# Kernel tuning notes

Hardware: AMD Instinct MI355X
Metric: run time of the kernel (lower is better)

Reference implementation:

```python
import jax, jax.numpy as jnp
import numpy as np

B, S, D, H = 2, 2048, 2048, 16
DH = D // H
FF = 4 * D
EPS = 1e-5


def setup_inputs() -> dict:
    key = jax.random.key(0)
    ks = jax.random.split(key, 8)
    sd = 0.02
    return {
        "hidden_states": jax.random.normal(ks[0], (B, S, D), jnp.float32),
        "ln1_w": jnp.ones((D,), jnp.float32),
        "ln1_b": jnp.zeros((D,), jnp.float32),
        "qkv_w": jax.random.normal(ks[1], (3 * D, D), jnp.float32) * sd,
        "qkv_b": jnp.zeros((3 * D,), jnp.float32),
        "dense_w": jax.random.normal(ks[2], (D, D), jnp.float32) * sd,
        "dense_b": jnp.zeros((D,), jnp.float32),
        "ln2_w": jnp.ones((D,), jnp.float32),
        "ln2_b": jnp.zeros((D,), jnp.float32),
        "fc1_w": jax.random.normal(ks[3], (FF, D), jnp.float32) * sd,
        "fc1_b": jnp.zeros((FF,), jnp.float32),
        "fc2_w": jax.random.normal(ks[4], (D, FF), jnp.float32) * sd,
        "fc2_b": jnp.zeros((D,), jnp.float32),
    }


def _layer_norm(x, w, b):
    mu = jnp.mean(x, axis=-1, keepdims=True)
    var = jnp.mean(jnp.square(x - mu), axis=-1, keepdims=True)
    return (x - mu) * jax.lax.rsqrt(var + EPS) * w + b


def _attention(x, qkv_w, qkv_b, dense_w, dense_b):
    qkv = x @ qkv_w.T + qkv_b  # [B,S,3D]
    q, k, v = jnp.split(qkv, 3, axis=-1)
    q = q.reshape(B, S, H, DH)
    k = k.reshape(B, S, H, DH)
    v = v.reshape(B, S, H, DH)
    scale = DH ** -0.5
    scores = jnp.einsum("bqhd,bkhd->bhqk", q, k) * scale
    causal = jnp.tril(jnp.ones((S, S), bool))
    scores = jnp.where(causal, scores, jnp.finfo(scores.dtype).min)
    probs = jax.nn.softmax(scores, axis=-1)
    out = jnp.einsum("bhqk,bkhd->bqhd", probs, v).reshape(B, S, D)
    return out @ dense_w.T + dense_b


def reference(hidden_states, ln1_w, ln1_b, qkv_w, qkv_b, dense_w, dense_b,
              ln2_w, ln2_b, fc1_w, fc1_b, fc2_w, fc2_b):
    residual = hidden_states
    x = _layer_norm(hidden_states, ln1_w, ln1_b)
    x = _attention(x, qkv_w, qkv_b, dense_w, dense_b) + residual
    residual = x
    h = _layer_norm(x, ln2_w, ln2_b)
    h = jax.nn.gelu(h @ fc1_w.T + fc1_b, approximate=False)
    h = h @ fc2_w.T + fc2_b
    return residual + h
```

## Files before the change

### kernel.cpp

```cpp
#include <hip/hip_runtime.h>
#include <hip/hip_bf16.h>

#define SEQ    2048
#define DMODEL 2048
#define NHEAD  16
#define DHEAD  128
#define TOK    4096
#define TD     6144
#define FFDIM  8192

typedef __attribute__((ext_vector_type(4)))  float f32x4;
typedef __attribute__((ext_vector_type(16))) float f32x16;
typedef __attribute__((ext_vector_type(8)))  short short8v;

__device__ __forceinline__ void async_ld16(const void* src, void* lds) {
  __builtin_amdgcn_global_load_lds((const __attribute__((address_space(1))) void*)src,
                                   (__attribute__((address_space(3))) void*)lds, 16, 0, 0);
}

__device__ __forceinline__ unsigned pk2(float a, float b) {
  union { __hip_bfloat16 h[2]; unsigned u; } p;
  p.h[0] = __float2bfloat16(a);
  p.h[1] = __float2bfloat16(b);
  return p.u;
}

__global__ __launch_bounds__(256) void f2bf_kernel(const float* __restrict__ in,
                                                   __hip_bfloat16* __restrict__ out, long n) {
  long i0 = ((long)blockIdx.x * 256 + threadIdx.x) * 8;
  long stride = (long)gridDim.x * 256 * 8;
  for (long i = i0; i < n; i += stride) {
    float4 a = *(const float4*)(in + i);
    float4 b = *(const float4*)(in + i + 4);
    union { __hip_bfloat16 h[8]; int4 v; } p;
    p.h[0] = __float2bfloat16(a.x); p.h[1] = __float2bfloat16(a.y);
    p.h[2] = __float2bfloat16(a.z); p.h[3] = __float2bfloat16(a.w);
    p.h[4] = __float2bfloat16(b.x); p.h[5] = __float2bfloat16(b.y);
    p.h[6] = __float2bfloat16(b.z); p.h[7] = __float2bfloat16(b.w);
    *(int4*)(out + i) = p.v;
  }
}

__global__ __launch_bounds__(256) void ln_kernel(const float* __restrict__ x,
                                                 const float* __restrict__ w,
                                                 const float* __restrict__ b,
                                                 __hip_bfloat16* __restrict__ out) {
  __shared__ float red[8];
  const int row = blockIdx.x;
  const int tid = threadIdx.x;
  const float* xr = x + (long)row * DMODEL;
  float4 v0 = ((const float4*)xr)[tid * 2];
  float4 v1 = ((const float4*)xr)[tid * 2 + 1];
  float s  = v0.x + v0.y + v0.z + v0.w + v1.x + v1.y + v1.z + v1.w;
  float ss = v0.x*v0.x + v0.y*v0.y + v0.z*v0.z + v0.w*v0.w
           + v1.x*v1.x + v1.y*v1.y + v1.z*v1.z + v1.w*v1.w;
  #pragma unroll
  for (int m = 1; m < 64; m <<= 1) { s += __shfl_xor(s, m, 64); ss += __shfl_xor(ss, m, 64); }
  if ((tid & 63) == 0) { red[tid >> 6] = s; red[4 + (tid >> 6)] = ss; }
  __syncthreads();
  s  = red[0] + red[1] + red[2] + red[3];
  ss = red[4] + red[5] + red[6] + red[7];
  const float mu = s * (1.0f / DMODEL);
  const float rs = rsqrtf(ss * (1.0f / DMODEL) - mu * mu + 1e-5f);
  float4 w0 = ((const float4*)w)[tid * 2], w1 = ((const float4*)w)[tid * 2 + 1];
  float4 b0 = ((const float4*)b)[tid * 2], b1 = ((const float4*)b)[tid * 2 + 1];
  union { __hip_bfloat16 h[8]; int4 v; } p;
  p.h[0] = __float2bfloat16((v0.x - mu) * rs * w0.x + b0.x);
  p.h[1] = __float2bfloat16((v0.y - mu) * rs * w0.y + b0.y);
  p.h[2] = __float2bfloat16((v0.z - mu) * rs * w0.z + b0.z);
  p.h[3] = __float2bfloat16((v0.w - mu) * rs * w0.w + b0.w);
  p.h[4] = __float2bfloat16((v1.x - mu) * rs * w1.x + b1.x);
  p.h[5] = __float2bfloat16((v1.y - mu) * rs * w1.y + b1.y);
  p.h[6] = __float2bfloat16((v1.z - mu) * rs * w1.z + b1.z);
  p.h[7] = __float2bfloat16((v1.w - mu) * rs * w1.w + b1.w);
  ((int4*)(out + (long)row * DMODEL))[tid] = p.v;
}

#define G2_BAR()    asm volatile("s_barrier" ::: "memory")
#define G2_BARLG()  asm volatile("s_barrier\ns_waitcnt lgkmcnt(0)" ::: "memory")
#define G2_VM4()    asm volatile("s_waitcnt vmcnt(4)\ns_barrier" ::: "memory")
#define G2_VM0()    asm volatile("s_waitcnt vmcnt(0)\ns_barrier" ::: "memory")

#define READ_A(BB, MH) \
  _Pragma("unroll") \
  for (int m = 0; m < 4; ++m) { \
    int row = wr * 128 + (MH) * 64 + m * 16 + l15; \
    _Pragma("unroll") \
    for (int kk = 0; kk < 2; ++kk) \
      af[m][kk] = *(const short8v*)((BB) + row * 128 + ((((kk << 2) | c16) ^ (row & 7)) << 4)); \
  }
#define MFMA_BLK(MH, NB) \
  __builtin_amdgcn_s_setprio(1); \
  _Pragma("unroll") \
  for (int m = 0; m < 4; ++m) \
    _Pragma("unroll") \
    for (int n = 0; n < 2; ++n) \
      _Pragma("unroll") \
      for (int kk = 0; kk < 2; ++kk) \
        acc[(MH) * 4 + m][(NB) + n] = __builtin_amdgcn_mfma_f32_16x16x32_bf16( \
            af[m][kk], bf[(NB) + n][kk], acc[(MH) * 4 + m][(NB) + n], 0, 0, 0); \
  __builtin_amdgcn_s_setprio(0);

#define READ_B128(BB) \
  _Pragma("unroll") \
  for (int n = 0; n < 2; ++n) { \
    int row = wc * 32 + n * 16 + l15; \
    _Pragma("unroll") \
    for (int kk = 0; kk < 2; ++kk) \
      bf[n][kk] = *(const short8v*)((BB) + 32768 + row * 128 + ((((kk << 2) | c16) ^ (row & 7)) << 4)); \
  }

template <int MODE>
__global__ __launch_bounds__(512, 2) void gemm128n(const __hip_bfloat16* __restrict__ A,
                                                   const __hip_bfloat16* __restrict__ B,
                                                   const float* __restrict__ bias,
                                                   const float* __restrict__ resid,
                                                   void* __restrict__ outp,
                                                   int N, long K) {
  __shared__ __align__(16) char lds[98304];
  const int tid = threadIdx.x;
  const int lane = tid & 63, w = tid >> 6;
  const int wr = w >> 2, wc = w & 3;
  const int l15 = lane & 15, c16 = lane >> 4;
  const int gx = gridDim.x;
  const int nwg = gx * (int)gridDim.y;
  const int lin = (int)blockIdx.y * gx + (int)blockIdx.x;
  const int cpx = nwg >> 3;
  const int swz = (lin & 7) * cpx + (lin >> 3);
  const long m0 = (long)(swz / gx) * 256;
  const long n0 = (long)(swz % gx) * 128;
  const int NT = (int)(K >> 6);
  const int NI = NT >> 1;

  auto stA2 = [&](int t, int par) {
    char* base = lds + (t & 1) * 49152;
    #pragma unroll
    for (int j = 0; j < 2; ++j) {
      int q = 2 * j + par;
      int row = q * 64 + (tid >> 3);
      long col = (long)t * 64 + (((tid & 7) ^ (row & 7)) << 3);
      async_ld16(A + (m0 + row) * K + col, base + q * 8192 + w * 1024);
    }
  };
  auto stB1 = [&](int t) {
    char* base = lds + (t & 1) * 49152 + 32768;
    #pragma unroll
    for (int j = 0; j < 2; ++j) {
      int row = j * 64 + (tid >> 3);
      long col = (long)t * 64 + (((tid & 7) ^ (row & 7)) << 3);
      async_ld16(B + (n0 + row) * K + col, base + j * 8192 + w * 1024);
    }
  };

  f32x4 acc[8][2] = {};
  short8v af[4][2], bf[2][2];
  const char* b0 = lds;
  const char* b1 = lds + 49152;

  stB1(0); stA2(0, 0); stA2(0, 1);
  stB1(1); stA2(1, 0);
  G2_VM4();

  for (int i = 0; i < NI; ++i) {
    const bool lastit = (i == NI - 1);
    READ_A(b0, 0); READ_B128(b0);
    stA2(2 * i + 1, 1);
    G2_BARLG(); MFMA_BLK(0, 0); G2_BAR();
    READ_A(b0, 1);
    if (!lastit) { stB1(2 * i + 2); stA2(2 * i + 2, 0); }
    G2_BARLG(); MFMA_BLK(1, 0);
    if (lastit) { G2_VM0(); } else { G2_VM4(); }
    READ_A(b1, 0); READ_B128(b1);
    if (!lastit) stA2(2 * i + 2, 1);
    G2_BARLG(); MFMA_BLK(0, 0); G2_BAR();
    READ_A(b1, 1);
    if (!lastit) { stB1(2 * i + 3); stA2(2 * i + 3, 0); }
    G2_BARLG(); MFMA_BLK(1, 0);
    if (lastit) { G2_BAR(); } else { G2_VM4(); }
  }

  const int colq = l15;
  const int rowq = c16 * 4;
  #pragma unroll
  for (int n = 0; n < 2; ++n) {
    long col = n0 + wc * 32 + n * 16 + colq;
    float bi = bias[col];
    #pragma unroll
    for (int mi = 0; mi < 8; ++mi) {
      long row0 = m0 + wr * 128 + mi * 16 + rowq;
      #pragma unroll
      for (int j = 0; j < 4; ++j) {
        long idx = (row0 + j) * (long)N + col;
        float v = acc[mi][n][j] + bi;
        if (MODE == 0) {
          ((__hip_bfloat16*)outp)[idx] = __float2bfloat16(v);
        } else if (MODE == 1) {
          ((float*)outp)[idx] = v + resid[idx];
        } else {
          float g = 0.5f * v * (1.0f + erff(v * 0.70710678118654752f));
          ((__hip_bfloat16*)outp)[idx] = __float2bfloat16(g);
        }
      }
    }
  }
}

#define QBLK 128
#define KVB  64
#define VSTR 144
#define KBYT 16384
#define VBYT (DHEAD * VSTR)
__global__ __launch_bounds__(256, 2) void attn_kernel(const __hip_bfloat16* __restrict__ qkv,
                                                      __hip_bfloat16* __restrict__ out) {
  __shared__ __align__(16) char smem[2 * KBYT + 2 * VBYT];
  const int tid = threadIdx.x, lane = tid & 63, wid = tid >> 6;
  const int l31 = lane & 31, hi = lane >> 5;
  const int bx = blockIdx.x;
  const int bh = blockIdx.y;
  const int bb = bh >> 4, h = bh & 15;
  const long rowbase = (long)bb * SEQ;
  const int qcol = h * DHEAD, kcol = DMODEL + h * DHEAD, vcol = 2 * DMODEL + h * DHEAD;

  const int kv0s = (tid >> 4) * 4;
  const int dh0s = (tid & 15) * 8;
  auto k_stage = [&](int t) {
    char* kb = smem + (t & 1) * KBYT;
    const long kvr = rowbase + (long)t * KVB;
    #pragma unroll
    for (int i = 0; i < 4; ++i) {
      int c = i * 256 + tid;
      int row = c >> 4, slot = c & 15;
      const void* src = qkv + (kvr + row) * TD + kcol + ((slot ^ (row & 7)) << 3);
      async_ld16(src, kb + i * 4096 + wid * 1024);
    }
  };
  auto v_load = [&](int t, int4* r) {
    const long kvr = rowbase + (long)t * KVB;
    #pragma unroll
    for (int i = 0; i < 4; ++i)
      r[i] = *(const int4*)(qkv + (kvr + kv0s + i) * TD + vcol + dh0s);
  };
  auto v_write = [&](int t, const int4* r) {
    char* vt = smem + 2 * KBYT + (t & 1) * VBYT;
    union { int4 v; unsigned short s[8]; } u0, u1, u2, u3;
    u0.v = r[0]; u1.v = r[1]; u2.v = r[2]; u3.v = r[3];
    #pragma unroll
    for (int dd = 0; dd < 8; ++dd) {
      int d = (dd + ((tid >> 1) & 7)) & 7;
      unsigned lo = (unsigned)u0.s[d] | ((unsigned)u1.s[d] << 16);
      unsigned hi2 = (unsigned)u2.s[d] | ((unsigned)u3.s[d] << 16);
      uint2 wv; wv.x = lo; wv.y = hi2;
      *(uint2*)(vt + (dh0s + d) * VSTR + kv0s * 2) = wv;
    }
  };

  #pragma unroll
  for (int mem = 0; mem < 2; ++mem) {
    const int qb = mem == 0 ? (15 - bx) : bx;
    const int q0 = qb * QBLK;
    const int qw0 = q0 + wid * 32;

    short8v qf[8];
    {
      const __hip_bfloat16* qp = qkv + (rowbase + qw0 + l31) * TD + qcol + hi * 8;
      #pragma unroll
      for (int kc = 0; kc < 8; ++kc) qf[kc] = *(const short8v*)(qp + kc * 16);
    }

    f32x16 o[4] = {};
    float m_ = -1e30f, l_ = 0.0f;
    const int nt = (q0 + QBLK) / KVB;

    {
      int4 vr[4];
      v_load(0, vr);
      k_stage(0);
      v_write(0, vr);
    }
    __syncthreads();

    for (int t = 0; t < nt; ++t) {
      int4 vr[4];
      const bool more = (t + 1 < nt);
      if (more) { v_load(t + 1, vr); k_stage(t + 1); }

      const int kv0 = t * KVB;
      if (kv0 <= qw0 + 31) {
        const char* Kb = smem + (t & 1) * KBYT;
        f32x16 s0 = {}, s1 = {};
        #pragma unroll
        for (int kc = 0; kc < 8; ++kc) {
          const int colb = kc * 32 + hi * 16;
          const int r0 = l31, r1 = 32 + l31;
          short8v k0 = *(const short8v*)(Kb + r0 * 256 + (colb ^ ((r0 & 7) << 4)));
          short8v k1 = *(const short8v*)(Kb + r1 * 256 + (colb ^ ((r0 & 7) << 4)));
          s0 = __builtin_amdgcn_mfma_f32_32x32x16_bf16(k0, qf[kc], s0, 0, 0, 0);
          s1 = __builtin_amdgcn_mfma_f32_32x32x16_bf16(k1, qf[kc], s1, 0, 0, 0);
        }
        const float scale = 0.08838834764831845f;
        float sv[32];
        #pragma unroll
        for (int r = 0; r < 16; ++r) { sv[r] = s0[r] * scale; sv[16 + r] = s1[r] * scale; }
        const int qg = qw0 + l31;
        if (kv0 + KVB - 1 > qw0) {
          #pragma unroll
          for (int r = 0; r < 16; ++r) {
            int kvr_ = kv0 + (r & 3) + 8 * (r >> 2) + 4 * hi;
            if (kvr_ > qg)      sv[r]      = -1e30f;
            if (kvr_ + 32 > qg) sv[16 + r] = -1e30f;
          }
        }
        float pmax = sv[0];
        #pragma unroll
        for (int r = 1; r < 32; ++r) pmax = fmaxf(pmax, sv[r]);
        pmax = fmaxf(pmax, __shfl_xor(pmax, 32, 64));
        float mn = fmaxf(m_, pmax);
        float alpha = __expf(m_ - mn);
        m_ = mn;
        l_ *= alpha;
        #pragma unroll
        for (int d = 0; d < 4; ++d)
          #pragma unroll
          for (int r = 0; r < 16; ++r) o[d][r] *= alpha;
        float rsum = 0.0f;
        #pragma unroll
        for (int r = 0; r < 32; ++r) { sv[r] = __expf(sv[r] - m_); rsum += sv[r]; }
        l_ += rsum + __shfl_xor(rsum, 32, 64);
        int pa_[4][4];
        #pragma unroll
        for (int kc = 0; kc < 4; ++kc) {
          int ba = 16 * (kc >> 1) + 8 * (kc & 1);
          unsigned wA0 = pk2(sv[ba + 0], sv[ba + 1]);
          unsigned wA1 = pk2(sv[ba + 2], sv[ba + 3]);
          unsigned wB0 = pk2(sv[ba + 4], sv[ba + 5]);
          unsigned wB1 = pk2(sv[ba + 6], sv[ba + 7]);
          unsigned z0 = (unsigned)__shfl_xor((int)(hi ? wA0 : wB0), 32, 64);
          unsigned z1 = (unsigned)__shfl_xor((int)(hi ? wA1 : wB1), 32, 64);
          pa_[kc][0] = hi ? (int)z0 : (int)wA0;
          pa_[kc][1] = hi ? (int)z1 : (int)wA1;
          pa_[kc][2] = hi ? (int)wB0 : (int)z0;
          pa_[kc][3] = hi ? (int)wB1 : (int)z1;
        }
        const char* Vt = smem + 2 * KBYT + (t & 1) * VBYT;
        #pragma unroll
        for (int dht = 0; dht < 4; ++dht) {
          const int dh = dht * 32 + l31;
          short8v vf[4];
          #pragma unroll
          for (int kc = 0; kc < 4; ++kc)
            vf[kc] = *(const short8v*)(Vt + dh * VSTR + kc * 32 + hi * 16);
          #pragma unroll
          for (int kc = 0; kc < 4; ++kc) {
            union { int i[4]; short8v v; } bv;
            bv.i[0] = pa_[kc][0]; bv.i[1] = pa_[kc][1];
            bv.i[2] = pa_[kc][2]; bv.i[3] = pa_[kc][3];
            o[dht] = __builtin_amdgcn_mfma_f32_32x32x16_bf16(vf[kc], bv.v, o[dht], 0, 0, 0);
          }
        }
      }
      if (more) v_write(t + 1, vr);
      __syncthreads();
    }

    const float linv = 1.0f / l_;
    const long orow = (rowbase + qw0 + l31) * DMODEL + h * DHEAD;
    #pragma unroll
    for (int dht = 0; dht < 4; ++dht)
      #pragma unroll
      for (int rg = 0; rg < 4; ++rg) {
        union { __hip_bfloat16 hh[4]; uint2 u; } pk;
        #pragma unroll
        for (int i = 0; i < 4; ++i) pk.hh[i] = __float2bfloat16(o[dht][rg * 4 + i] * linv);
        *(uint2*)(out + orow + dht * 32 + 8 * rg + 4 * hi) = pk.u;
      }
  }
}

extern "C" void kernel_launch(void* const* d_in, const int* in_sizes, int n_in,
                              void* d_out, int out_size, void* d_ws, size_t ws_size,
                              hipStream_t stream) {
  const float* hidden  = (const float*)d_in[0];
  const float* ln1w    = (const float*)d_in[1];
  const float* ln1b    = (const float*)d_in[2];
  const float* qkvw    = (const float*)d_in[3];
  const float* qkvb    = (const float*)d_in[4];
  const float* densew  = (const float*)d_in[5];
  const float* denseb  = (const float*)d_in[6];
  const float* ln2w    = (const float*)d_in[7];
  const float* ln2b    = (const float*)d_in[8];
  const float* fc1w    = (const float*)d_in[9];
  const float* fc1b    = (const float*)d_in[10];
  const float* fc2w    = (const float*)d_in[11];
  const float* fc2b    = (const float*)d_in[12];

  char* ws = (char*)d_ws;
  size_t off = 0;
  auto alloc = [&](size_t bytes) { char* p = ws + off; off += (bytes + 255) & ~(size_t)255; return p; };
  __hip_bfloat16* xbf    = (__hip_bfloat16*)alloc((size_t)TOK * DMODEL * 2);
  __hip_bfloat16* wqkv   = (__hip_bfloat16*)alloc((size_t)TD * DMODEL * 2);
  __hip_bfloat16* wdense = (__hip_bfloat16*)alloc((size_t)DMODEL * DMODEL * 2);
  __hip_bfloat16* wfc1   = (__hip_bfloat16*)alloc((size_t)FFDIM * DMODEL * 2);
  __hip_bfloat16* wfc2   = (__hip_bfloat16*)alloc((size_t)DMODEL * FFDIM * 2);
  __hip_bfloat16* big    = (__hip_bfloat16*)alloc((size_t)TOK * FFDIM * 2);
  float*          x2     = (float*)alloc((size_t)TOK * DMODEL * 4);
  __hip_bfloat16* qkvbuf  = big;
  __hip_bfloat16* attnout = big + (size_t)TOK * TD;
  __hip_bfloat16* gelubuf = big;

  f2bf_kernel<<<1024, 256, 0, stream>>>(qkvw,   wqkv,   (long)TD * DMODEL);
  f2bf_kernel<<<1024, 256, 0, stream>>>(densew, wdense, (long)DMODEL * DMODEL);
  f2bf_kernel<<<1024, 256, 0, stream>>>(fc1w,   wfc1,   (long)FFDIM * DMODEL);
  f2bf_kernel<<<1024, 256, 0, stream>>>(fc2w,   wfc2,   (long)DMODEL * FFDIM);

  ln_kernel<<<TOK, 256, 0, stream>>>(hidden, ln1w, ln1b, xbf);
  gemm128n<0><<<dim3(TD / 128, TOK / 256), 512, 0, stream>>>(xbf, wqkv, qkvb, nullptr, qkvbuf, TD, DMODEL);
  attn_kernel<<<dim3(8, 2 * NHEAD), 256, 0, stream>>>(qkvbuf, attnout);
  gemm128n<1><<<dim3(DMODEL / 128, TOK / 256), 512, 0, stream>>>(attnout, wdense, denseb, hidden, x2, DMODEL, DMODEL);
  ln_kernel<<<TOK, 256, 0, stream>>>(x2, ln2w, ln2b, xbf);
  gemm128n<2><<<dim3(FFDIM / 128, TOK / 256), 512, 0, stream>>>(xbf, wfc1, fc1b, nullptr, gelubuf, FFDIM, DMODEL);
  gemm128n<1><<<dim3(DMODEL / 128, TOK / 256), 512, 0, stream>>>(gelubuf, wfc2, fc2b, x2, (float*)d_out, DMODEL, FFDIM);
}
```

Baseline: 667.7 us.

## Double-buffer GEMM register fragments to overlap LDS reads with MFMA

```diff
diff --git a/kernel.cpp b/kernel.cpp
--- a/kernel.cpp
+++ b/kernel.cpp
@@ -76,20 +76,27 @@
   ((int4*)(out + (long)row * DMODEL))[tid] = p.v;
 }
 
-#define G2_BAR()    asm volatile("s_barrier" ::: "memory")
-#define G2_BARLG()  asm volatile("s_barrier\ns_waitcnt lgkmcnt(0)" ::: "memory")
-#define G2_VM4()    asm volatile("s_waitcnt vmcnt(4)\ns_barrier" ::: "memory")
-#define G2_VM0()    asm volatile("s_waitcnt vmcnt(0)\ns_barrier" ::: "memory")
-
-#define READ_A(BB, MH) \
+#define VMBAR(N) asm volatile("s_waitcnt vmcnt(" #N ")\ns_barrier" ::: "memory")
+#define LGK(N)   do { asm volatile("s_waitcnt lgkmcnt(" #N ")" ::: "memory"); \
+                      __builtin_amdgcn_sched_barrier(0); } while (0)
+
+#define RA_READ_A(DST, BB, MH) \
   _Pragma("unroll") \
   for (int m = 0; m < 4; ++m) { \
     int row = wr * 128 + (MH) * 64 + m * 16 + l15; \
     _Pragma("unroll") \
     for (int kk = 0; kk < 2; ++kk) \
-      af[m][kk] = *(const short8v*)((BB) + row * 128 + ((((kk << 2) | c16) ^ (row & 7)) << 4)); \
-  }
-#define MFMA_BLK(MH, NB) \
+      DST[m][kk] = *(const short8v*)((BB) + row * 128 + ((((kk << 2) | c16) ^ (row & 7)) << 4)); \
+  }
+#define RA_READ_B(DST, BB) \
+  _Pragma("unroll") \
+  for (int n = 0; n < 2; ++n) { \
+    int row = wc * 32 + n * 16 + l15; \
+    _Pragma("unroll") \
+    for (int kk = 0; kk < 2; ++kk) \
+      DST[n][kk] = *(const short8v*)((BB) + 32768 + row * 128 + ((((kk << 2) | c16) ^ (row & 7)) << 4)); \
+  }
+#define RA_MFMA(AF, BF, MH) \
   __builtin_amdgcn_s_setprio(1); \
   _Pragma("unroll") \
   for (int m = 0; m < 4; ++m) \
@@ -97,26 +104,17 @@
     for (int n = 0; n < 2; ++n) \
       _Pragma("unroll") \
       for (int kk = 0; kk < 2; ++kk) \
-        acc[(MH) * 4 + m][(NB) + n] = __builtin_amdgcn_mfma_f32_16x16x32_bf16( \
-            af[m][kk], bf[(NB) + n][kk], acc[(MH) * 4 + m][(NB) + n], 0, 0, 0); \
+        acc[(MH) * 4 + m][n] = __builtin_amdgcn_mfma_f32_16x16x32_bf16( \
+            AF[m][kk], BF[n][kk], acc[(MH) * 4 + m][n], 0, 0, 0); \
   __builtin_amdgcn_s_setprio(0);
 
-#define READ_B128(BB) \
-  _Pragma("unroll") \
-  for (int n = 0; n < 2; ++n) { \
-    int row = wc * 32 + n * 16 + l15; \
-    _Pragma("unroll") \
-    for (int kk = 0; kk < 2; ++kk) \
-      bf[n][kk] = *(const short8v*)((BB) + 32768 + row * 128 + ((((kk << 2) | c16) ^ (row & 7)) << 4)); \
-  }
-
 template <int MODE>
-__global__ __launch_bounds__(512, 2) void gemm128n(const __hip_bfloat16* __restrict__ A,
-                                                   const __hip_bfloat16* __restrict__ B,
-                                                   const float* __restrict__ bias,
-                                                   const float* __restrict__ resid,
-                                                   void* __restrict__ outp,
-                                                   int N, long K) {
+__global__ __launch_bounds__(512, 2) void gemm128ra(const __hip_bfloat16* __restrict__ A,
+                                                    const __hip_bfloat16* __restrict__ B,
+                                                    const float* __restrict__ bias,
+                                                    const float* __restrict__ resid,
+                                                    void* __restrict__ outp,
+                                                    int N, long K) {
   __shared__ __align__(16) char lds[98304];
   const int tid = threadIdx.x;
   const int lane = tid & 63, w = tid >> 6;
@@ -153,30 +151,48 @@
   };
 
   f32x4 acc[8][2] = {};
-  short8v af[4][2], bf[2][2];
+  short8v afA[4][2], afB[4][2], bfA[2][2], bfB[2][2];
   const char* b0 = lds;
   const char* b1 = lds + 49152;
 
   stB1(0); stA2(0, 0); stA2(0, 1);
   stB1(1); stA2(1, 0);
-  G2_VM4();
+  asm volatile("s_waitcnt vmcnt(4)\ns_barrier" ::: "memory");
+  RA_READ_A(afA, b0, 0); RA_READ_B(bfA, b0);
 
   for (int i = 0; i < NI; ++i) {
-    const bool lastit = (i == NI - 1);
-    READ_A(b0, 0); READ_B128(b0);
-    stA2(2 * i + 1, 1);
-    G2_BARLG(); MFMA_BLK(0, 0); G2_BAR();
-    READ_A(b0, 1);
-    if (!lastit) { stB1(2 * i + 2); stA2(2 * i + 2, 0); }
-    G2_BARLG(); MFMA_BLK(1, 0);
-    if (lastit) { G2_VM0(); } else { G2_VM4(); }
-    READ_A(b1, 0); READ_B128(b1);
-    if (!lastit) stA2(2 * i + 2, 1);
-    G2_BARLG(); MFMA_BLK(0, 0); G2_BAR();
-    READ_A(b1, 1);
-    if (!lastit) { stB1(2 * i + 3); stA2(2 * i + 3, 0); }
-    G2_BARLG(); MFMA_BLK(1, 0);
-    if (lastit) { G2_BAR(); } else { G2_VM4(); }
+    const bool last = (i == NI - 1);
+    const int c = 2 * i + 1, e = 2 * i + 2, g = 2 * i + 3;
+
+    VMBAR(4);
+    RA_READ_A(afB, b0, 1);
+    stA2(c, 1);
+    LGK(8);
+    RA_MFMA(afA, bfA, 0);
+
+    VMBAR(2);
+    RA_READ_A(afA, b1, 0);
+    RA_READ_B(bfB, b1);
+    if (!last) { stB1(e); stA2(e, 0); }
+    LGK(12);
+    RA_MFMA(afB, bfA, 1);
+
+    if (!last) { VMBAR(4); } else { VMBAR(0); }
+    RA_READ_A(afB, b1, 1);
+    if (!last) stA2(e, 1);
+    LGK(8);
+    RA_MFMA(afA, bfB, 0);
+
+    if (!last) {
+      VMBAR(2);
+      RA_READ_A(afA, b0, 0);
+      RA_READ_B(bfA, b0);
+      stB1(g); stA2(g, 0);
+      LGK(12);
+    } else {
+      LGK(0);
+    }
+    RA_MFMA(afB, bfB, 1);
   }
 
   const int colq = l15;
@@ -413,10 +429,10 @@
   f2bf_kernel<<<1024, 256, 0, stream>>>(fc2w,   wfc2,   (long)DMODEL * FFDIM);
 
   ln_kernel<<<TOK, 256, 0, stream>>>(hidden, ln1w, ln1b, xbf);
-  gemm128n<0><<<dim3(TD / 128, TOK / 256), 512, 0, stream>>>(xbf, wqkv, qkvb, nullptr, qkvbuf, TD, DMODEL);
+  gemm128ra<0><<<dim3(TD / 128, TOK / 256), 512, 0, stream>>>(xbf, wqkv, qkvb, nullptr, qkvbuf, TD, DMODEL);
   attn_kernel<<<dim3(8, 2 * NHEAD), 256, 0, stream>>>(qkvbuf, attnout);
-  gemm128n<1><<<dim3(DMODEL / 128, TOK / 256), 512, 0, stream>>>(attnout, wdense, denseb, hidden, x2, DMODEL, DMODEL);
+  gemm128ra<1><<<dim3(DMODEL / 128, TOK / 256), 512, 0, stream>>>(attnout, wdense, denseb, hidden, x2, DMODEL, DMODEL);
   ln_kernel<<<TOK, 256, 0, stream>>>(x2, ln2w, ln2b, xbf);
-  gemm128n<2><<<dim3(FFDIM / 128, TOK / 256), 512, 0, stream>>>(xbf, wfc1, fc1b, nullptr, gelubuf, FFDIM, DMODEL);
-  gemm128n<1><<<dim3(DMODEL / 128, TOK / 256), 512, 0, stream>>>(gelubuf, wfc2, fc2b, x2, (float*)d_out, DMODEL, FFDIM);
-}
+  gemm128ra<2><<<dim3(FFDIM / 128, TOK / 256), 512, 0, stream>>>(xbf, wfc1, fc1b, nullptr, gelubuf, FFDIM, DMODEL);
+  gemm128ra<1><<<dim3(DMODEL / 128, TOK / 256), 512, 0, stream>>>(gelubuf, wfc2, fc2b, x2, (float*)d_out, DMODEL, FFDIM);
+}
```

Result: no change. 656.9 us (-1.6%).
